# Performance work log

Hardware: AMD Instinct MI355X
Metric: run time of the kernel (lower is better)

The kernel has to match this reference:

```python
import jax, jax.numpy as jnp
import numpy as np

N_NODES = 100000
N_EDGES = 1600000
F_IN = 128
F_OUT = 32
HEADS = 8
ALPHA = 0.2  # LeakyReLU slope


def setup_inputs() -> dict:
    key = jax.random.key(0)
    ks = jax.random.split(key, 7)
    x = jax.random.normal(ks[0], (N_NODES, F_IN), dtype=jnp.float32)
    row = jnp.sort(jax.random.randint(ks[1], (N_EDGES,), 0, N_NODES, dtype=jnp.int32))
    col = jax.random.randint(ks[2], (N_EDGES,), 0, N_NODES, dtype=jnp.int32)
    kernels = jax.random.normal(ks[3], (HEADS, F_IN, F_OUT), dtype=jnp.float32) * 0.1
    att_self = jax.random.normal(ks[4], (HEADS, F_OUT), dtype=jnp.float32) * 0.1
    att_neigh = jax.random.normal(ks[5], (HEADS, F_OUT), dtype=jnp.float32) * 0.1
    biases = jax.random.normal(ks[6], (HEADS, F_OUT), dtype=jnp.float32) * 0.1
    return {"x": x, "row": row, "col": col, "kernels": kernels,
            "att_self": att_self, "att_neigh": att_neigh, "biases": biases}


def reference(x, row, col, kernels, att_self, att_neigh, biases):
    # GraphAttention (GAT), eval mode (dropout inactive), concat over heads.
    N = x.shape[0]
    outs = []
    for h in range(kernels.shape[0]):  # fixed small head loop
        feat = x @ kernels[h]                     # [N, F_OUT]
        a_s = feat @ att_self[h]                  # [N]
        a_n = feat @ att_neigh[h]                 # [N]
        e = a_s[row] + a_n[col]                   # [E] edge logits (SDDMM)
        e = jnp.where(e > 0, e, ALPHA * e)        # LeakyReLU(0.2)
        # row-wise (destination-node) sparse softmax, numerically stable
        m = jax.ops.segment_max(e, row, num_segments=N)
        ex = jnp.exp(e - m[row])
        denom = jax.ops.segment_sum(ex, row, num_segments=N)
        alpha = ex / denom[row]                   # [E]
        # SpMM: out[i] = sum_{e: row[e]=i} alpha[e] * feat[col[e]]
        msg = alpha[:, None] * feat[col]          # [E, F_OUT]
        out = jax.ops.segment_sum(msg, row, num_segments=N) + biases[h]
        outs.append(out)
    return jnp.concatenate(outs, axis=1)          # [N, HEADS*F_OUT]
```

## Files before the change

### kernel.cpp

```cpp
#include <hip/hip_runtime.h>
#include <hip/hip_bf16.h>
#include <math.h>


#define F_IN   128
#define F_ALL  256
#define HEADS  8
#define F_OUT  32
#define ALPHA  0.2f
#define CHUNK  128

using f32x4  = __attribute__((ext_vector_type(4))) float;
using bf16x8 = __attribute__((ext_vector_type(8))) short;
using u16x8  = __attribute__((ext_vector_type(8))) unsigned short;

static __device__ __forceinline__ unsigned short f32_to_bf16(float f) {
  union { float f; unsigned u; } v; v.f = f;
  unsigned r = v.u + 0x7FFF + ((v.u >> 16) & 1);
  return (unsigned short)(r >> 16);
}
static __device__ __forceinline__ float bf16_lo(unsigned d) {
  return __uint_as_float(d << 16);
}
static __device__ __forceinline__ float bf16_hi(unsigned d) {
  return __uint_as_float(d & 0xffff0000u);
}

__global__ __launch_bounds__(256) void prep(const float* __restrict__ x,
                                            const float* __restrict__ kern,
                                            const float* __restrict__ att_s,
                                            const float* __restrict__ att_n,
                                            const int* __restrict__ row,
                                            unsigned short* __restrict__ xb,
                                            unsigned short* __restrict__ Wt,
                                            float* __restrict__ ws,
                                            float* __restrict__ wn,
                                            int* __restrict__ ptr,
                                            int total_x8, int N, int E) {
  int id = blockIdx.x * 256 + threadIdx.x;
  if (id < total_x8) {
    const float4* x4 = reinterpret_cast<const float4*>(x);
    float4 v0 = x4[(size_t)id * 2], v1 = x4[(size_t)id * 2 + 1];
    u16x8 o;
    o[0] = f32_to_bf16(v0.x); o[1] = f32_to_bf16(v0.y);
    o[2] = f32_to_bf16(v0.z); o[3] = f32_to_bf16(v0.w);
    o[4] = f32_to_bf16(v1.x); o[5] = f32_to_bf16(v1.y);
    o[6] = f32_to_bf16(v1.z); o[7] = f32_to_bf16(v1.w);
    *reinterpret_cast<u16x8*>(xb + (size_t)id * 8) = o;
  }
  if (id < F_ALL * F_IN) {
    int c = id >> 7, k = id & 127;
    Wt[id] = f32_to_bf16(kern[(size_t)(c >> 5) * (F_IN * F_OUT) + k * F_OUT + (c & 31)]);
  }
  if (id < 2 * HEADS * F_IN) {
    int which = id >> 10;
    int hk = id & 1023;
    int h = hk >> 7, k = hk & 127;
    const float* att = which ? att_n : att_s;
    float s = 0.f;
#pragma unroll
    for (int f = 0; f < F_OUT; ++f)
      s += kern[(size_t)h * (F_IN * F_OUT) + k * F_OUT + f] * att[h * F_OUT + f];
    (which ? wn : ws)[hk] = s;
  }
  if (id <= N) {
    int lo = 0, hi = E;
    while (lo < hi) {
      int mid = (lo + hi) >> 1;
      if (row[mid] < id) lo = mid + 1; else hi = mid;
    }
    ptr[id] = lo;
  }
}

__global__ __launch_bounds__(256) void a_proj_w(const float* __restrict__ x,
                                                const float* __restrict__ ws,
                                                const float* __restrict__ wn,
                                                float* __restrict__ a_s,
                                                float* __restrict__ a_n, int N) {
  const int l = threadIdx.x & 63;
  const int o = l & 15, q = l >> 4;
  const int wid    = (blockIdx.x * 256 + threadIdx.x) >> 6;
  const int nwaves = (gridDim.x * 256) >> 6;

  const float* wrow = (o < 8 ? ws + o * F_IN : wn + (o - 8) * F_IN) + q * 32;
  float4 wv[8];
#pragma unroll
  for (int i = 0; i < 8; i++) wv[i] = reinterpret_cast<const float4*>(wrow)[i];

  for (int n = wid; n < N; n += nwaves) {
    const float4* xr = reinterpret_cast<const float4*>(x + (size_t)n * F_IN + q * 32);
    float acc = 0.f;
#pragma unroll
    for (int i = 0; i < 8; i++) {
      float4 xv = xr[i];
      acc += xv.x * wv[i].x + xv.y * wv[i].y + xv.z * wv[i].z + xv.w * wv[i].w;
    }
    acc += __shfl_xor(acc, 16);
    acc += __shfl_xor(acc, 32);
    if (l < 16) {
      if (o < 8) a_s[n * HEADS + o] = acc;
      else       a_n[n * HEADS + (o - 8)] = acc;
    }
  }
}

__global__ __launch_bounds__(256) void feat_gemm_mfma(
    const unsigned short* __restrict__ xb,
    const unsigned short* __restrict__ Wt,
    unsigned short* __restrict__ featb,
    int N) {
  const int t  = threadIdx.x;
  const int w  = t >> 6;
  const int l  = t & 63;
  const int lr = l & 15;
  const int lq = l >> 4;
  const int n0 = blockIdx.x * 64 + w * 16;

  f32x4 acc[16];
#pragma unroll
  for (int ct = 0; ct < 16; ++ct) acc[ct] = (f32x4){0.f, 0.f, 0.f, 0.f};

  int ar = n0 + lr; if (ar >= N) ar = N - 1;
  const unsigned short* xrow = xb + (size_t)ar * F_IN + lq * 8;
  bf16x8 afr[4];
#pragma unroll
  for (int kc = 0; kc < 4; ++kc)
    afr[kc] = *reinterpret_cast<const bf16x8*>(xrow + kc * 32);

#pragma unroll
  for (int ct = 0; ct < 16; ++ct) {
    const unsigned short* wrow = Wt + (size_t)(ct * 16 + lr) * F_IN + lq * 8;
#pragma unroll
    for (int kc = 0; kc < 4; ++kc) {
      bf16x8 bfr = *reinterpret_cast<const bf16x8*>(wrow + kc * 32);
      acc[ct] = __builtin_amdgcn_mfma_f32_16x16x32_bf16(afr[kc], bfr, acc[ct], 0, 0, 0);
    }
  }

#pragma unroll
  for (int r = 0; r < 4; ++r) {
    int n = n0 + lq * 4 + r;
    if (n < N) {
#pragma unroll
      for (int ct = 0; ct < 16; ++ct)
        featb[(size_t)n * F_ALL + ct * 16 + lr] = f32_to_bf16(acc[ct][r]);
    }
  }
}

__global__ __launch_bounds__(256) void gat_scatter(
    const unsigned short* __restrict__ featb,
    const float* __restrict__ a_s, const float* __restrict__ a_n,
    const int* __restrict__ col, const int* __restrict__ ptr,
    const float* __restrict__ biases, float* __restrict__ out, int N) {
  __shared__ float wlds[HEADS][CHUNK + 1];
  __shared__ int   clds[CHUNK];
  const int n = blockIdx.x;
  const int t = threadIdx.x;
  const int h = t >> 5;
  const int f = t & 31;
  const int start = ptr[n];
  const int deg   = ptr[n + 1] - start;

  if (deg == 0) { out[(size_t)n * F_ALL + t] = biases[t]; return; }
  const float as = a_s[n * HEADS + h];
  const unsigned* fu32 = reinterpret_cast<const unsigned*>(featb);

  if (deg <= 32) {
    int c = 0; float ex = 0.f;
    if (f < deg) {
      c = col[start + f];
      float e0 = as + a_n[c * HEADS + h];
      e0 = e0 > 0.f ? e0 : ALPHA * e0;
      ex = __expf(e0);
    }
    float sm = ex;
#pragma unroll
    for (int m = 16; m; m >>= 1) sm += __shfl_xor(sm, m);
    const float inv = 1.0f / sm;

    const int q = f & 15, p = f >> 4;
    const int dbase = h * 16 + q;
    float a0 = 0.f, a1 = 0.f, b0 = 0.f, b1 = 0.f;
    int e = 0;
    for (; e + 4 <= deg; e += 4) {
      int   ca = __shfl(c,  e + p,     32);
      float wa = __shfl(ex, e + p,     32);
      int   cb = __shfl(c,  e + 2 + p, 32);
      float wb = __shfl(ex, e + 2 + p, 32);
      unsigned da = fu32[ca * 128 + dbase];
      unsigned db = fu32[cb * 128 + dbase];
      a0 = fmaf(wa, bf16_lo(da), a0);
      a1 = fmaf(wa, bf16_hi(da), a1);
      b0 = fmaf(wb, bf16_lo(db), b0);
      b1 = fmaf(wb, bf16_hi(db), b1);
    }
    for (; e < deg; e += 2) {
      int idx = e + p;
      int cl  = idx < deg ? idx : 0;
      int   ca = __shfl(c,  cl, 32);
      float wa = __shfl(ex, cl, 32);
      if (idx >= deg) wa = 0.f;
      unsigned da = fu32[ca * 128 + dbase];
      a0 = fmaf(wa, bf16_lo(da), a0);
      a1 = fmaf(wa, bf16_hi(da), a1);
    }
    a0 += b0; a1 += b1;
    a0 += __shfl_xor(a0, 16);
    a1 += __shfl_xor(a1, 16);
    if (p == 0) {
      const float2 bv = *reinterpret_cast<const float2*>(&biases[h * F_OUT + q * 2]);
      float2 o;
      o.x = a0 * inv + bv.x;
      o.y = a1 * inv + bv.y;
      *reinterpret_cast<float2*>(&out[(size_t)n * F_ALL + h * F_OUT + q * 2]) = o;
    }
    return;
  }

  float sm = 0.f;
  for (int e = f; e < deg; e += 32) {
    int cc = col[start + e];
    float e0 = as + a_n[cc * HEADS + h];
    e0 = e0 > 0.f ? e0 : ALPHA * e0;
    float x2 = __expf(e0);
    sm += x2;
    if (e < CHUNK) {
      wlds[h][e] = x2;
      if (h == 0) clds[e] = cc;
    }
  }
#pragma unroll
  for (int m = 16; m; m >>= 1) sm += __shfl_xor(sm, m);
  const float inv = 1.0f / sm;

  __syncthreads();

  float ac0 = 0.f, ac1 = 0.f, ac2 = 0.f, ac3 = 0.f;
  const int base = h * F_OUT + f;
  {
    const int cn = deg < CHUNK ? deg : CHUNK;
    int e = 0;
    for (; e + 4 <= cn; e += 4) {
      int ca = clds[e], cb = clds[e + 1], cc = clds[e + 2], cd = clds[e + 3];
      float wa = wlds[h][e],     wb = wlds[h][e + 1];
      float wc = wlds[h][e + 2], wd = wlds[h][e + 3];
      ac0 = fmaf(wa, __uint_as_float((unsigned)featb[(size_t)ca * F_ALL + base] << 16), ac0);
      ac1 = fmaf(wb, __uint_as_float((unsigned)featb[(size_t)cb * F_ALL + base] << 16), ac1);
      ac2 = fmaf(wc, __uint_as_float((unsigned)featb[(size_t)cc * F_ALL + base] << 16), ac2);
      ac3 = fmaf(wd, __uint_as_float((unsigned)featb[(size_t)cd * F_ALL + base] << 16), ac3);
    }
    for (; e < cn; ++e)
      ac0 = fmaf(wlds[h][e],
                 __uint_as_float((unsigned)featb[(size_t)clds[e] * F_ALL + base] << 16), ac0);
  }
  for (int cs = CHUNK; cs < deg; cs += CHUNK) {
    __syncthreads();
    int cn = deg - cs; if (cn > CHUNK) cn = CHUNK;
    for (int e = f; e < cn; e += 32) {
      int cc = col[start + cs + e];
      if (h == 0) clds[e] = cc;
      float e0 = as + a_n[cc * HEADS + h];
      e0 = e0 > 0.f ? e0 : ALPHA * e0;
      wlds[h][e] = __expf(e0);
    }
    __syncthreads();
    for (int e = 0; e < cn; ++e)
      ac0 = fmaf(wlds[h][e],
                 __uint_as_float((unsigned)featb[(size_t)clds[e] * F_ALL + base] << 16), ac0);
  }
  out[(size_t)n * F_ALL + t] = (ac0 + ac1 + ac2 + ac3) * inv + biases[t];
}

extern "C" void kernel_launch(void* const* d_in, const int* in_sizes, int n_in,
                              void* d_out, int out_size, void* d_ws, size_t ws_size,
                              hipStream_t stream) {
  const float* x      = (const float*)d_in[0];
  const int*   row    = (const int*)d_in[1];
  const int*   col    = (const int*)d_in[2];
  const float* kern   = (const float*)d_in[3];
  const float* att_s  = (const float*)d_in[4];
  const float* att_n  = (const float*)d_in[5];
  const float* biases = (const float*)d_in[6];

  const int N = in_sizes[0] / F_IN;
  const int E = in_sizes[1];

  unsigned short* featb = (unsigned short*)d_ws;
  unsigned short* xb    = featb + (size_t)N * F_ALL;
  unsigned short* Wt    = xb + (size_t)N * F_IN;
  float* ws  = (float*)(Wt + F_ALL * F_IN);
  float* wn  = ws + HEADS * F_IN;
  float* a_s = wn + HEADS * F_IN;
  float* a_n = a_s + (size_t)N * HEADS;
  int*   ptr = (int*)(a_n + (size_t)N * HEADS);
  float* out = (float*)d_out;

  const int total_x8 = N * F_IN / 8;
  hipLaunchKernelGGL(prep, dim3((total_x8 + 255) / 256), dim3(256), 0, stream,
                     x, kern, att_s, att_n, row, xb, Wt, ws, wn, ptr, total_x8, N, E);
  hipLaunchKernelGGL(a_proj_w, dim3(2048), dim3(256), 0, stream,
                     x, ws, wn, a_s, a_n, N);
  hipLaunchKernelGGL(feat_gemm_mfma, dim3((N + 63) / 64), dim3(256), 0, stream,
                     xb, Wt, featb, N);
  hipLaunchKernelGGL(gat_scatter, dim3(N), dim3(256), 0, stream,
                     featb, a_s, a_n, col, ptr, biases, out, N);
}
```

Baseline: 309.3 us.

## Merge GEMM and attention projection launch, pack two nodes per scatter block

Fuses the MFMA feature GEMM and the attention-logit projection into one launch, split by block index. The GEMM now swaps operands so each lane holds four consecutive features and writes them as packed bf16 pairs using v_cvt_pk_bf16_f32 with 8-byte stores. The scatter kernel processes two nodes per 256-thread block, with 16 lanes per head each owning two features. Its high-degree path drops the LDS chunking and syncthreads in favour of a single streaming loop that recomputes edge weights, which trades extra col/a_n reads for fewer barriers and less LDS.

Result: faster. 277.2 us (-10.3%).

```diff
diff --git a/kernel.cpp b/kernel.cpp
--- a/kernel.cpp
+++ b/kernel.cpp
@@ -8,7 +8,6 @@
 #define HEADS  8
 #define F_OUT  32
 #define ALPHA  0.2f
-#define CHUNK  128
 
 using f32x4  = __attribute__((ext_vector_type(4))) float;
 using bf16x8 = __attribute__((ext_vector_type(8))) short;
@@ -18,6 +17,11 @@
   union { float f; unsigned u; } v; v.f = f;
   unsigned r = v.u + 0x7FFF + ((v.u >> 16) & 1);
   return (unsigned short)(r >> 16);
+}
+static __device__ __forceinline__ unsigned cvt_pk_bf16(float lo, float hi) {
+  unsigned r;
+  asm("v_cvt_pk_bf16_f32 %0, %1, %2" : "=v"(r) : "v"(lo), "v"(hi));
+  return r;
 }
 static __device__ __forceinline__ float bf16_lo(unsigned d) {
   return __uint_as_float(d << 16);
@@ -73,22 +77,66 @@
   }
 }
 
-__global__ __launch_bounds__(256) void a_proj_w(const float* __restrict__ x,
-                                                const float* __restrict__ ws,
-                                                const float* __restrict__ wn,
-                                                float* __restrict__ a_s,
-                                                float* __restrict__ a_n, int N) {
-  const int l = threadIdx.x & 63;
+__global__ __launch_bounds__(256) void gemm_aproj(
+    const unsigned short* __restrict__ xb,
+    const unsigned short* __restrict__ Wt,
+    const float* __restrict__ x,
+    const float* __restrict__ ws, const float* __restrict__ wn,
+    unsigned short* __restrict__ featb,
+    float* __restrict__ a_s, float* __restrict__ a_n,
+    int N, int gemm_blocks, int aproj_waves) {
+  const int t = threadIdx.x;
+
+  if ((int)blockIdx.x < gemm_blocks) {
+    const int w  = t >> 6;
+    const int l  = t & 63;
+    const int lr = l & 15;
+    const int lq = l >> 4;
+    const int n0 = blockIdx.x * 64 + w * 16;
+
+    f32x4 acc[16];
+#pragma unroll
+    for (int ct = 0; ct < 16; ++ct) acc[ct] = (f32x4){0.f, 0.f, 0.f, 0.f};
+
+    int ar = n0 + lr; if (ar >= N) ar = N - 1;
+    const unsigned short* xrow = xb + (size_t)ar * F_IN + lq * 8;
+    bf16x8 xfr[4];
+#pragma unroll
+    for (int kc = 0; kc < 4; ++kc)
+      xfr[kc] = *reinterpret_cast<const bf16x8*>(xrow + kc * 32);
+
+#pragma unroll
+    for (int ct = 0; ct < 16; ++ct) {
+      const unsigned short* wrow = Wt + (size_t)(ct * 16 + lr) * F_IN + lq * 8;
+#pragma unroll
+      for (int kc = 0; kc < 4; ++kc) {
+        bf16x8 wfr = *reinterpret_cast<const bf16x8*>(wrow + kc * 32);
+        acc[ct] = __builtin_amdgcn_mfma_f32_16x16x32_bf16(wfr, xfr[kc], acc[ct], 0, 0, 0);
+      }
+    }
+    if (n0 + lr < N) {
+      unsigned short* frow = featb + (size_t)ar * F_ALL + lq * 4;
+#pragma unroll
+      for (int ct = 0; ct < 16; ++ct) {
+        uint2 v;
+        v.x = cvt_pk_bf16(acc[ct][0], acc[ct][1]);
+        v.y = cvt_pk_bf16(acc[ct][2], acc[ct][3]);
+        *reinterpret_cast<uint2*>(frow + ct * 16) = v;
+      }
+    }
+    return;
+  }
+
+  const int l = t & 63;
   const int o = l & 15, q = l >> 4;
-  const int wid    = (blockIdx.x * 256 + threadIdx.x) >> 6;
-  const int nwaves = (gridDim.x * 256) >> 6;
+  const int wid = (((int)blockIdx.x - gemm_blocks) * 256 + t) >> 6;
 
   const float* wrow = (o < 8 ? ws + o * F_IN : wn + (o - 8) * F_IN) + q * 32;
   float4 wv[8];
 #pragma unroll
   for (int i = 0; i < 8; i++) wv[i] = reinterpret_cast<const float4*>(wrow)[i];
 
-  for (int n = wid; n < N; n += nwaves) {
+  for (int n = wid; n < N; n += aproj_waves) {
     const float4* xr = reinterpret_cast<const float4*>(x + (size_t)n * F_IN + q * 32);
     float acc = 0.f;
 #pragma unroll
@@ -105,172 +153,113 @@
   }
 }
 
-__global__ __launch_bounds__(256) void feat_gemm_mfma(
-    const unsigned short* __restrict__ xb,
-    const unsigned short* __restrict__ Wt,
-    unsigned short* __restrict__ featb,
-    int N) {
-  const int t  = threadIdx.x;
-  const int w  = t >> 6;
-  const int l  = t & 63;
-  const int lr = l & 15;
-  const int lq = l >> 4;
-  const int n0 = blockIdx.x * 64 + w * 16;
-
-  f32x4 acc[16];
-#pragma unroll
-  for (int ct = 0; ct < 16; ++ct) acc[ct] = (f32x4){0.f, 0.f, 0.f, 0.f};
-
-  int ar = n0 + lr; if (ar >= N) ar = N - 1;
-  const unsigned short* xrow = xb + (size_t)ar * F_IN + lq * 8;
-  bf16x8 afr[4];
-#pragma unroll
-  for (int kc = 0; kc < 4; ++kc)
-    afr[kc] = *reinterpret_cast<const bf16x8*>(xrow + kc * 32);
-
-#pragma unroll
-  for (int ct = 0; ct < 16; ++ct) {
-    const unsigned short* wrow = Wt + (size_t)(ct * 16 + lr) * F_IN + lq * 8;
-#pragma unroll
-    for (int kc = 0; kc < 4; ++kc) {
-      bf16x8 bfr = *reinterpret_cast<const bf16x8*>(wrow + kc * 32);
-      acc[ct] = __builtin_amdgcn_mfma_f32_16x16x32_bf16(afr[kc], bfr, acc[ct], 0, 0, 0);
-    }
-  }
-
-#pragma unroll
-  for (int r = 0; r < 4; ++r) {
-    int n = n0 + lq * 4 + r;
-    if (n < N) {
-#pragma unroll
-      for (int ct = 0; ct < 16; ++ct)
-        featb[(size_t)n * F_ALL + ct * 16 + lr] = f32_to_bf16(acc[ct][r]);
-    }
-  }
-}
-
 __global__ __launch_bounds__(256) void gat_scatter(
     const unsigned short* __restrict__ featb,
     const float* __restrict__ a_s, const float* __restrict__ a_n,
     const int* __restrict__ col, const int* __restrict__ ptr,
     const float* __restrict__ biases, float* __restrict__ out, int N) {
-  __shared__ float wlds[HEADS][CHUNK + 1];
-  __shared__ int   clds[CHUNK];
-  const int n = blockIdx.x;
-  const int t = threadIdx.x;
-  const int h = t >> 5;
-  const int f = t & 31;
+  const int t    = threadIdx.x;
+  const int n    = blockIdx.x * 2 + (t >> 7);
+  if (n >= N) return;
+  const int tl   = t & 127;
+  const int q    = tl & 15;
+  const int h    = ((tl >> 5) << 1) | ((tl >> 4) & 1);
+  const int obase = h * F_OUT + q * 2;
+
   const int start = ptr[n];
   const int deg   = ptr[n + 1] - start;
 
-  if (deg == 0) { out[(size_t)n * F_ALL + t] = biases[t]; return; }
+  const float2 bv = *reinterpret_cast<const float2*>(&biases[obase]);
+  if (deg == 0) {
+    *reinterpret_cast<float2*>(&out[(size_t)n * F_ALL + obase]) = bv;
+    return;
+  }
+
   const float as = a_s[n * HEADS + h];
   const unsigned* fu32 = reinterpret_cast<const unsigned*>(featb);
+  const int dbase = h * 16 + q;
 
   if (deg <= 32) {
-    int c = 0; float ex = 0.f;
-    if (f < deg) {
-      c = col[start + f];
-      float e0 = as + a_n[c * HEADS + h];
-      e0 = e0 > 0.f ? e0 : ALPHA * e0;
-      ex = __expf(e0);
-    }
-    float sm = ex;
-#pragma unroll
-    for (int m = 16; m; m >>= 1) sm += __shfl_xor(sm, m);
+    int c1 = 0, c2 = 0;
+    float ex1 = 0.f, ex2 = 0.f;
+    if (q < deg) {
+      c1 = col[start + q];
+      float v = as + a_n[c1 * HEADS + h];
+      v = v > 0.f ? v : ALPHA * v;
+      ex1 = __expf(v);
+    }
+    if (q + 16 < deg) {
+      c2 = col[start + q + 16];
+      float v = as + a_n[c2 * HEADS + h];
+      v = v > 0.f ? v : ALPHA * v;
+      ex2 = __expf(v);
+    }
+    float sm = ex1 + ex2;
+#pragma unroll
+    for (int m = 1; m <= 8; m <<= 1) sm += __shfl_xor(sm, m);
     const float inv = 1.0f / sm;
 
-    const int q = f & 15, p = f >> 4;
-    const int dbase = h * 16 + q;
     float a0 = 0.f, a1 = 0.f, b0 = 0.f, b1 = 0.f;
-    int e = 0;
-    for (; e + 4 <= deg; e += 4) {
-      int   ca = __shfl(c,  e + p,     32);
-      float wa = __shfl(ex, e + p,     32);
-      int   cb = __shfl(c,  e + 2 + p, 32);
-      float wb = __shfl(ex, e + 2 + p, 32);
-      unsigned da = fu32[ca * 128 + dbase];
-      unsigned db = fu32[cb * 128 + dbase];
+    const int d1 = ((deg < 16 ? deg : 16) + 1) & ~1;
+    for (int e = 0; e < d1; e += 2) {
+      int   ca = __shfl(c1,  e,     16);
+      float wa = __shfl(ex1, e,     16);
+      int   cb = __shfl(c1,  e + 1, 16);
+      float wb = __shfl(ex1, e + 1, 16);
+      unsigned da = fu32[(size_t)ca * 128 + dbase];
+      unsigned db = fu32[(size_t)cb * 128 + dbase];
       a0 = fmaf(wa, bf16_lo(da), a0);
       a1 = fmaf(wa, bf16_hi(da), a1);
       b0 = fmaf(wb, bf16_lo(db), b0);
       b1 = fmaf(wb, bf16_hi(db), b1);
     }
-    for (; e < deg; e += 2) {
-      int idx = e + p;
-      int cl  = idx < deg ? idx : 0;
-      int   ca = __shfl(c,  cl, 32);
-      float wa = __shfl(ex, cl, 32);
-      if (idx >= deg) wa = 0.f;
-      unsigned da = fu32[ca * 128 + dbase];
-      a0 = fmaf(wa, bf16_lo(da), a0);
-      a1 = fmaf(wa, bf16_hi(da), a1);
-    }
-    a0 += b0; a1 += b1;
-    a0 += __shfl_xor(a0, 16);
-    a1 += __shfl_xor(a1, 16);
-    if (p == 0) {
-      const float2 bv = *reinterpret_cast<const float2*>(&biases[h * F_OUT + q * 2]);
-      float2 o;
-      o.x = a0 * inv + bv.x;
-      o.y = a1 * inv + bv.y;
-      *reinterpret_cast<float2*>(&out[(size_t)n * F_ALL + h * F_OUT + q * 2]) = o;
-    }
+    if (deg > 16) {
+      const int d2 = (deg - 16 + 1) & ~1;
+      for (int e = 0; e < d2; e += 2) {
+        int   ca = __shfl(c2,  e,     16);
+        float wa = __shfl(ex2, e,     16);
+        int   cb = __shfl(c2,  e + 1, 16);
+        float wb = __shfl(ex2, e + 1, 16);
+        unsigned da = fu32[(size_t)ca * 128 + dbase];
+        unsigned db = fu32[(size_t)cb * 128 + dbase];
+        a0 = fmaf(wa, bf16_lo(da), a0);
+        a1 = fmaf(wa, bf16_hi(da), a1);
+        b0 = fmaf(wb, bf16_lo(db), b0);
+        b1 = fmaf(wb, bf16_hi(db), b1);
+      }
+    }
+    float2 o;
+    o.x = (a0 + b0) * inv + bv.x;
+    o.y = (a1 + b1) * inv + bv.y;
+    *reinterpret_cast<float2*>(&out[(size_t)n * F_ALL + obase]) = o;
     return;
   }
 
   float sm = 0.f;
-  for (int e = f; e < deg; e += 32) {
-    int cc = col[start + e];
-    float e0 = as + a_n[cc * HEADS + h];
-    e0 = e0 > 0.f ? e0 : ALPHA * e0;
-    float x2 = __expf(e0);
-    sm += x2;
-    if (e < CHUNK) {
-      wlds[h][e] = x2;
-      if (h == 0) clds[e] = cc;
-    }
-  }
-#pragma unroll
-  for (int m = 16; m; m >>= 1) sm += __shfl_xor(sm, m);
+  for (int e = q; e < deg; e += 16) {
+    int c = col[start + e];
+    float v = as + a_n[c * HEADS + h];
+    v = v > 0.f ? v : ALPHA * v;
+    sm += __expf(v);
+  }
+#pragma unroll
+  for (int m = 1; m <= 8; m <<= 1) sm += __shfl_xor(sm, m);
   const float inv = 1.0f / sm;
 
-  __syncthreads();
-
-  float ac0 = 0.f, ac1 = 0.f, ac2 = 0.f, ac3 = 0.f;
-  const int base = h * F_OUT + f;
-  {
-    const int cn = deg < CHUNK ? deg : CHUNK;
-    int e = 0;
-    for (; e + 4 <= cn; e += 4) {
-      int ca = clds[e], cb = clds[e + 1], cc = clds[e + 2], cd = clds[e + 3];
-      float wa = wlds[h][e],     wb = wlds[h][e + 1];
-      float wc = wlds[h][e + 2], wd = wlds[h][e + 3];
-      ac0 = fmaf(wa, __uint_as_float((unsigned)featb[(size_t)ca * F_ALL + base] << 16), ac0);
-      ac1 = fmaf(wb, __uint_as_float((unsigned)featb[(size_t)cb * F_ALL + base] << 16), ac1);
-      ac2 = fmaf(wc, __uint_as_float((unsigned)featb[(size_t)cc * F_ALL + base] << 16), ac2);
-      ac3 = fmaf(wd, __uint_as_float((unsigned)featb[(size_t)cd * F_ALL + base] << 16), ac3);
-    }
-    for (; e < cn; ++e)
-      ac0 = fmaf(wlds[h][e],
-                 __uint_as_float((unsigned)featb[(size_t)clds[e] * F_ALL + base] << 16), ac0);
-  }
-  for (int cs = CHUNK; cs < deg; cs += CHUNK) {
-    __syncthreads();
-    int cn = deg - cs; if (cn > CHUNK) cn = CHUNK;
-    for (int e = f; e < cn; e += 32) {
-      int cc = col[start + cs + e];
-      if (h == 0) clds[e] = cc;
-      float e0 = as + a_n[cc * HEADS + h];
-      e0 = e0 > 0.f ? e0 : ALPHA * e0;
-      wlds[h][e] = __expf(e0);
-    }
-    __syncthreads();
-    for (int e = 0; e < cn; ++e)
-      ac0 = fmaf(wlds[h][e],
-                 __uint_as_float((unsigned)featb[(size_t)clds[e] * F_ALL + base] << 16), ac0);
-  }
-  out[(size_t)n * F_ALL + t] = (ac0 + ac1 + ac2 + ac3) * inv + biases[t];
+  float f0 = 0.f, f1 = 0.f;
+  for (int e = 0; e < deg; ++e) {
+    int c = col[start + e];
+    float v = as + a_n[c * HEADS + h];
+    v = v > 0.f ? v : ALPHA * v;
+    float wv = __expf(v);
+    unsigned d = fu32[(size_t)c * 128 + dbase];
+    f0 = fmaf(wv, bf16_lo(d), f0);
+    f1 = fmaf(wv, bf16_hi(d), f1);
+  }
+  float2 o;
+  o.x = f0 * inv + bv.x;
+  o.y = f1 * inv + bv.y;
+  *reinterpret_cast<float2*>(&out[(size_t)n * F_ALL + obase]) = o;
 }
 
 extern "C" void kernel_launch(void* const* d_in, const int* in_sizes, int n_in,
@@ -297,13 +286,15 @@
   int*   ptr = (int*)(a_n + (size_t)N * HEADS);
   float* out = (float*)d_out;
 
-  const int total_x8 = N * F_IN / 8;
+  const int total_x8    = N * F_IN / 8;
+  const int gemm_blocks = (N + 63) / 64;
+  const int aproj_blocks = 1024;
+  const int aproj_waves  = aproj_blocks * 4;
+
   hipLaunchKernelGGL(prep, dim3((total_x8 + 255) / 256), dim3(256), 0, stream,
                      x, kern, att_s, att_n, row, xb, Wt, ws, wn, ptr, total_x8, N, E);
-  hipLaunchKernelGGL(a_proj_w, dim3(2048), dim3(256), 0, stream,
-                     x, ws, wn, a_s, a_n, N);
-  hipLaunchKernelGGL(feat_gemm_mfma, dim3((N + 63) / 64), dim3(256), 0, stream,
-                     xb, Wt, featb, N);
-  hipLaunchKernelGGL(gat_scatter, dim3(N), dim3(256), 0, stream,
+  hipLaunchKernelGGL(gemm_aproj, dim3(gemm_blocks + aproj_blocks), dim3(256), 0, stream,
+                     xb, Wt, x, ws, wn, featb, a_s, a_n, N, gemm_blocks, aproj_waves);
+  hipLaunchKernelGGL(gat_scatter, dim3((N + 1) / 2), dim3(256), 0, stream,
                      featb, a_s, a_n, col, ptr, biases, out, N);
 }
```
